# Optimization experiments

Hardware: AMD Instinct MI355X
Metric: run time of the kernel (lower is better)

The kernel has to match this reference:

```python
import jax, jax.numpy as jnp
import numpy as np

NUM_HEADS = 16

def setup_inputs() -> dict:
    key = jax.random.key(0)
    ks = jax.random.split(key, 7)
    B, N, D = 2, 2048, 1024
    x = jax.random.normal(ks[0], (B, N, D), dtype=jnp.float32)
    gamma = jax.random.uniform(ks[1], (B, NUM_HEADS), dtype=jnp.float32)
    dist_matrix = jax.random.uniform(ks[2], (N, N), dtype=jnp.float32)
    W_qkv = jax.random.normal(ks[3], (D, 3 * D), dtype=jnp.float32) * (D ** -0.5)
    b_qkv = jnp.zeros((3 * D,), dtype=jnp.float32)
    W_proj = jax.random.normal(ks[4], (D, D), dtype=jnp.float32) * (D ** -0.5)
    b_proj = jnp.zeros((D,), dtype=jnp.float32)
    return {"x": x, "gamma": gamma, "dist_matrix": dist_matrix,
            "W_qkv": W_qkv, "b_qkv": b_qkv, "W_proj": W_proj, "b_proj": b_proj}

def reference(x, gamma, dist_matrix, W_qkv, b_qkv, W_proj, b_proj):
    B, N, D = x.shape
    H = NUM_HEADS
    hd = D // H
    scale = D ** -0.5  # standard_scale=False -> dim**-0.5
    # qkv projection: [B,N,3D] -> [3,B,H,N,hd]
    qkv = (x @ W_qkv + b_qkv).reshape(B, N, 3, H, hd).transpose(2, 0, 3, 1, 4)
    q, k, v = qkv[0], qkv[1], qkv[2]
    # scores with zoom bias: [B,H,N,N]
    scores = jnp.einsum('bhnd,bhmd->bhnm', q, k) * scale
    scores = scores - gamma[:, :, None, None] * dist_matrix[None, None, :, :]
    attn = jax.nn.softmax(scores, axis=-1)
    out = jnp.einsum('bhnm,bhmd->bhnd', attn, v)  # [B,H,N,hd]
    out = out.transpose(0, 2, 1, 3).reshape(B, N, D)
    return out @ W_proj + b_proj
```

## Files before the change

kernel.cpp:

```cpp
#include <hip/hip_runtime.h>
#include <cstdint>
#include <cstddef>

#define HD 64
#define NH 16
#define BATCH 2
#define SEQ 2048
#define DIM 1024
#define SCALE 0.03125f
#define LOG2E 1.4426950408889634f
#define QSCALE (SCALE * LOG2E)
#define NT (SEQ / 64)

typedef short bf16x8 __attribute__((ext_vector_type(8)));
typedef float f32x4 __attribute__((ext_vector_type(4)));
typedef float f32x16 __attribute__((ext_vector_type(16)));
typedef unsigned u32x4 __attribute__((ext_vector_type(4)));

#define GL16(gp, lp) __builtin_amdgcn_global_load_lds( \
    (const __attribute__((address_space(1))) unsigned int*)(gp), \
    (__attribute__((address_space(3))) unsigned int*)(lp), 16, 0, 0)

static __device__ __forceinline__ unsigned short f2bf(float f) {
  union { float f; unsigned u; } a; a.f = f;
  unsigned r = a.u + 0x7fffu + ((a.u >> 16) & 1u);
  return (unsigned short)(r >> 16);
}

static __device__ __forceinline__ f32x4 zero4() {
  f32x4 z; z[0] = 0.f; z[1] = 0.f; z[2] = 0.f; z[3] = 0.f; return z;
}

__global__ void convert_x(const float* __restrict__ in, unsigned short* __restrict__ out, int n4) {
  int i = blockIdx.x * blockDim.x + threadIdx.x;
  if (i < n4) {
    float4 v = reinterpret_cast<const float4*>(in)[i];
    ushort4 o;
    o.x = f2bf(v.x); o.y = f2bf(v.y); o.z = f2bf(v.z); o.w = f2bf(v.w);
    reinterpret_cast<ushort4*>(out)[i] = o;
  }
}

__global__ void transpose_convert(const float* __restrict__ in, unsigned short* __restrict__ out,
                                  int R, int C) {
  __shared__ float tile[32][33];
  int bx = blockIdx.x * 32;
  int by = blockIdx.y * 32;
  int tx = threadIdx.x, ty = threadIdx.y;
  #pragma unroll
  for (int i = 0; i < 32; i += 8)
    tile[ty + i][tx] = in[(size_t)(by + ty + i) * C + bx + tx];
  __syncthreads();
  #pragma unroll
  for (int i = 0; i < 32; i += 8)
    out[(size_t)(bx + ty + i) * R + by + tx] = f2bf(tile[tx][ty + i]);
}

__global__ __launch_bounds__(256) void gemm128(
    const unsigned short* __restrict__ A, const unsigned short* __restrict__ Bt,
    const float* __restrict__ bias, int K, int mode,
    unsigned short* __restrict__ qo, unsigned short* __restrict__ ko,
    unsigned short* __restrict__ vo, float* __restrict__ outf) {
  __shared__ __attribute__((aligned(16))) unsigned short As[128 * 64];
  __shared__ __attribute__((aligned(16))) unsigned short Bs[128 * 64];
  const int tid = threadIdx.x;
  const int lane = tid & 63, w = tid >> 6;
  const int lo = lane & 15, hi = lane >> 4;
  const int wm = w >> 1, wn = w & 1;
  const int m0 = blockIdx.y * 128, n0 = blockIdx.x * 128;
  const int srow = tid >> 3, scol = (tid & 7) * 8;
  const unsigned short* abase = A + (size_t)(m0 + srow) * K + scol;
  const unsigned short* bbase = Bt + (size_t)(n0 + srow) * K + scol;

  f32x4 acc[4][4];
  #pragma unroll
  for (int mr = 0; mr < 4; ++mr)
    #pragma unroll
    for (int nr = 0; nr < 4; ++nr) acc[mr][nr] = zero4();

  const int nkt = K / 64;
  for (int kt = 0; kt < nkt; ++kt) {
    const unsigned short* ak = abase + kt * 64;
    const unsigned short* bk = bbase + kt * 64;
    #pragma unroll
    for (int i = 0; i < 4; ++i) {
      GL16(ak + (size_t)(32 * i) * K, &As[(w * 64 + 256 * i) * 8]);
      GL16(bk + (size_t)(32 * i) * K, &Bs[(w * 64 + 256 * i) * 8]);
    }
    __syncthreads();
    __builtin_amdgcn_s_setprio(1);
    #pragma unroll
    for (int kc = 0; kc < 2; ++kc) {
      bf16x8 af[4], bfr[4];
      #pragma unroll
      for (int mr = 0; mr < 4; ++mr)
        af[mr] = *reinterpret_cast<const bf16x8*>(
            &As[(wm * 64 + mr * 16 + lo) * 64 + kc * 32 + hi * 8]);
      #pragma unroll
      for (int nr = 0; nr < 4; ++nr)
        bfr[nr] = *reinterpret_cast<const bf16x8*>(
            &Bs[(wn * 64 + nr * 16 + lo) * 64 + kc * 32 + hi * 8]);
      #pragma unroll
      for (int mr = 0; mr < 4; ++mr)
        #pragma unroll
        for (int nr = 0; nr < 4; ++nr)
          acc[mr][nr] = __builtin_amdgcn_mfma_f32_16x16x32_bf16(af[mr], bfr[nr], acc[mr][nr], 0, 0, 0);
    }
    __builtin_amdgcn_s_setprio(0);
    __syncthreads();
  }

  #pragma unroll
  for (int nr = 0; nr < 4; ++nr) {
    const int gcol = n0 + wn * 64 + nr * 16 + lo;
    const float bv = bias[gcol];
    #pragma unroll
    for (int mr = 0; mr < 4; ++mr)
      #pragma unroll
      for (int j = 0; j < 4; ++j) {
        const int grow = m0 + wm * 64 + mr * 16 + hi * 4 + j;
        float val = acc[mr][nr][j] + bv;
        if (mode == 0) {
          int which = gcol >> 10;
          int hh = (gcol >> 6) & 15;
          int d = gcol & 63;
          int bb = grow >> 11;
          int n = grow & 2047;
          if (which == 0) {
            qo[((size_t)(bb * NH + hh) * SEQ + n) * HD + d] = f2bf(val * QSCALE);
          } else if (which == 1) {
            ko[((size_t)(bb * NH + hh) * SEQ + n) * HD + d] = f2bf(val);
          } else {
            vo[((size_t)(bb * NH + hh) * HD + d) * SEQ + n] = f2bf(val);
          }
        } else {
          outf[(size_t)grow * DIM + gcol] = val;
        }
      }
  }
}

__global__ __launch_bounds__(256, 2) void attn_kernel(
    const unsigned short* __restrict__ qb, const unsigned short* __restrict__ kb,
    const unsigned short* __restrict__ vtb, const float* __restrict__ gamma,
    const float* __restrict__ dist, unsigned short* __restrict__ ab) {
  __shared__ __attribute__((aligned(16))) unsigned short Ks[2][64 * 64];
  __shared__ __attribute__((aligned(16))) unsigned short Vt[2][64 * 64];
  const int tid = threadIdx.x;
  const int lane = tid & 63;
  const int w = tid >> 6;
  const int q5 = lane & 31;
  const int h5 = lane >> 5;
  const int idx = blockIdx.x;
  const int bh = idx & 31;
  const int qt = idx >> 5;
  const int b = bh >> 4, h = bh & 15;
  const int qrow0 = qt * 128 + w * 32;
  const float g2 = gamma[bh] * LOG2E;

  const size_t base = (size_t)bh * SEQ * HD;
  const size_t vtbase = (size_t)bh * HD * SEQ;

  bf16x8 qf[4];
  #pragma unroll
  for (int ks = 0; ks < 4; ++ks)
    qf[ks] = *reinterpret_cast<const bf16x8*>(
        &qb[base + (size_t)(qrow0 + q5) * HD + ks * 16 + h5 * 8]);

  const float* drow = dist + (size_t)(qrow0 + q5) * SEQ + 4 * h5;

  f32x16 o[2];
  #pragma unroll
  for (int i = 0; i < 16; ++i) { o[0][i] = 0.f; o[1][i] = 0.f; }
  float m_run = -INFINITY;
  float l_run = 0.f;

  const int srow = tid >> 3;
  const int schunk = (tid & 7) ^ (srow & 7);
  const unsigned short* ksrc0 = kb + base + (size_t)srow * HD + schunk * 8;
  const unsigned short* ksrc1 = ksrc0 + (size_t)32 * HD;
  const unsigned short* vsrc0 = vtb + vtbase + (size_t)srow * SEQ + schunk * 8;
  const unsigned short* vsrc1 = vsrc0 + (size_t)32 * SEQ;

  f32x4 dv[2][4];
  #pragma unroll
  for (int blk = 0; blk < 2; ++blk)
    #pragma unroll
    for (int rp = 0; rp < 4; ++rp)
      dv[blk][rp] = *reinterpret_cast<const f32x4*>(drow + 32 * blk + 8 * rp);

  GL16(ksrc0, &Ks[0][w * 512]);
  GL16(ksrc1, &Ks[0][2048 + w * 512]);
  GL16(vsrc0, &Vt[0][w * 512]);
  GL16(vsrc1, &Vt[0][2048 + w * 512]);
  __syncthreads();

  for (int mt = 0; mt < NT; ++mt) {
    const int cur = mt & 1;
    if (mt + 1 < NT) {
      const int m1 = (mt + 1) * 64;
      GL16(ksrc0 + (size_t)m1 * HD, &Ks[cur ^ 1][w * 512]);
      GL16(ksrc1 + (size_t)m1 * HD, &Ks[cur ^ 1][2048 + w * 512]);
      GL16(vsrc0 + m1, &Vt[cur ^ 1][w * 512]);
      GL16(vsrc1 + m1, &Vt[cur ^ 1][2048 + w * 512]);
    }

    f32x16 s[2];
    #pragma unroll
    for (int i = 0; i < 16; ++i) { s[0][i] = 0.f; s[1][i] = 0.f; }
    __builtin_amdgcn_s_setprio(1);
    #pragma unroll
    for (int blk = 0; blk < 2; ++blk)
      #pragma unroll
      for (int ks = 0; ks < 4; ++ks) {
        bf16x8 kf = *reinterpret_cast<const bf16x8*>(
            &Ks[cur][(blk * 32 + q5) * 64 + ((ks * 2 + h5) ^ (q5 & 7)) * 8]);
        s[blk] = __builtin_amdgcn_mfma_f32_32x32x16_bf16(kf, qf[ks], s[blk], 0, 0, 0);
      }
    __builtin_amdgcn_s_setprio(0);

    float mx[8];
    #pragma unroll
    for (int blk = 0; blk < 2; ++blk)
      #pragma unroll
      for (int rp = 0; rp < 4; ++rp) {
        float v0 = __builtin_fmaf(-g2, dv[blk][rp][0], s[blk][rp * 4 + 0]);
        float v1 = __builtin_fmaf(-g2, dv[blk][rp][1], s[blk][rp * 4 + 1]);
        float v2 = __builtin_fmaf(-g2, dv[blk][rp][2], s[blk][rp * 4 + 2]);
        float v3 = __builtin_fmaf(-g2, dv[blk][rp][3], s[blk][rp * 4 + 3]);
        s[blk][rp * 4 + 0] = v0; s[blk][rp * 4 + 1] = v1;
        s[blk][rp * 4 + 2] = v2; s[blk][rp * 4 + 3] = v3;
        mx[blk * 4 + rp] = fmaxf(fmaxf(v0, v1), fmaxf(v2, v3));
      }
    float pm = fmaxf(fmaxf(fmaxf(mx[0], mx[1]), fmaxf(mx[2], mx[3])),
                     fmaxf(fmaxf(mx[4], mx[5]), fmaxf(mx[6], mx[7])));
    pm = fmaxf(pm, __shfl_xor(pm, 32, 64));

    if (mt + 1 < NT) {
      const float* dn = drow + (mt + 1) * 64;
      #pragma unroll
      for (int blk = 0; blk < 2; ++blk)
        #pragma unroll
        for (int rp = 0; rp < 4; ++rp)
          dv[blk][rp] = *reinterpret_cast<const f32x4*>(dn + 32 * blk + 8 * rp);
    }

    if (!__all(pm <= m_run + 8.0f)) {
      float mn = fmaxf(m_run, pm);
      float corr = exp2f(m_run - mn);
      m_run = mn;
      l_run *= corr;
      #pragma unroll
      for (int i = 0; i < 16; ++i) { o[0][i] *= corr; o[1][i] *= corr; }
    }

    float psum = 0.f;
    unsigned u[2][4][2];
    #pragma unroll
    for (int blk = 0; blk < 2; ++blk)
      #pragma unroll
      for (int rp = 0; rp < 4; ++rp) {
        float p0 = exp2f(s[blk][rp * 4 + 0] - m_run);
        float p1 = exp2f(s[blk][rp * 4 + 1] - m_run);
        float p2 = exp2f(s[blk][rp * 4 + 2] - m_run);
        float p3 = exp2f(s[blk][rp * 4 + 3] - m_run);
        psum += (p0 + p1) + (p2 + p3);
        asm("v_cvt_pk_bf16_f32 %0, %1, %2" : "=v"(u[blk][rp][0]) : "v"(p0), "v"(p1));
        asm("v_cvt_pk_bf16_f32 %0, %1, %2" : "=v"(u[blk][rp][1]) : "v"(p2), "v"(p3));
      }
    psum += __shfl_xor(psum, 32, 64);
    l_run += psum;

    unsigned pu[4][4];
    #pragma unroll
    for (int blk = 0; blk < 2; ++blk)
      #pragma unroll
      for (int jp = 0; jp < 2; ++jp) {
        unsigned a0 = u[blk][0][jp], b0 = u[blk][1][jp];
        asm("v_permlane32_swap_b32 %0, %1" : "+v"(a0), "+v"(b0));
        pu[2 * blk][jp] = a0; pu[2 * blk][2 + jp] = b0;
        unsigned a1 = u[blk][2][jp], b1 = u[blk][3][jp];
        asm("v_permlane32_swap_b32 %0, %1" : "+v"(a1), "+v"(b1));
        pu[2 * blk + 1][jp] = a1; pu[2 * blk + 1][2 + jp] = b1;
      }

    __builtin_amdgcn_s_setprio(1);
    #pragma unroll
    for (int ks = 0; ks < 4; ++ks) {
      u32x4 t; t[0] = pu[ks][0]; t[1] = pu[ks][1]; t[2] = pu[ks][2]; t[3] = pu[ks][3];
      bf16x8 pf = __builtin_bit_cast(bf16x8, t);
      #pragma unroll
      for (int db = 0; db < 2; ++db) {
        bf16x8 vtf = *reinterpret_cast<const bf16x8*>(
            &Vt[cur][(db * 32 + q5) * 64 + ((ks * 2 + h5) ^ (q5 & 7)) * 8]);
        o[db] = __builtin_amdgcn_mfma_f32_32x32x16_bf16(vtf, pf, o[db], 0, 0, 0);
      }
    }
    __builtin_amdgcn_s_setprio(0);

    __syncthreads();
  }

  {
    float rl = 1.0f / l_run;
    size_t row = (size_t)b * SEQ + qrow0 + q5;
    unsigned short* obase = ab + row * DIM + h * HD + 4 * h5;
    #pragma unroll
    for (int db = 0; db < 2; ++db)
      #pragma unroll
      for (int rp = 0; rp < 4; ++rp) {
        ushort4 w4;
        w4.x = f2bf(o[db][rp * 4 + 0] * rl);
        w4.y = f2bf(o[db][rp * 4 + 1] * rl);
        w4.z = f2bf(o[db][rp * 4 + 2] * rl);
        w4.w = f2bf(o[db][rp * 4 + 3] * rl);
        *reinterpret_cast<ushort4*>(&obase[db * 32 + 8 * rp]) = w4;
      }
  }
}

extern "C" void kernel_launch(void* const* d_in, const int* in_sizes, int n_in,
                              void* d_out, int out_size, void* d_ws, size_t ws_size,
                              hipStream_t stream) {
  const float* x     = (const float*)d_in[0];
  const float* gamma = (const float*)d_in[1];
  const float* dist  = (const float*)d_in[2];
  const float* Wqkv  = (const float*)d_in[3];
  const float* bqkv  = (const float*)d_in[4];
  const float* Wproj = (const float*)d_in[5];
  const float* bproj = (const float*)d_in[6];
  float* out = (float*)d_out;

  char* ws = (char*)d_ws;
  unsigned short* xb     = (unsigned short*)(ws);
  unsigned short* wqkvt  = (unsigned short*)(ws + 8388608);
  unsigned short* wprojt = (unsigned short*)(ws + 14680064);
  unsigned short* qbuf   = (unsigned short*)(ws + 16777216);
  unsigned short* kbuf   = (unsigned short*)(ws + 25165824);
  unsigned short* vtbuf  = (unsigned short*)(ws + 33554432);
  unsigned short* abuf   = (unsigned short*)(ws + 41943040);

  convert_x<<<4096, 256, 0, stream>>>(x, xb, (BATCH * SEQ * DIM) / 4);
  transpose_convert<<<dim3(96, 32), dim3(32, 8), 0, stream>>>(Wqkv, wqkvt, DIM, 3 * DIM);
  transpose_convert<<<dim3(32, 32), dim3(32, 8), 0, stream>>>(Wproj, wprojt, DIM, DIM);
  gemm128<<<dim3(24, 32), 256, 0, stream>>>(xb, wqkvt, bqkv, DIM, 0, qbuf, kbuf, vtbuf, nullptr);
  attn_kernel<<<(SEQ / 128) * BATCH * NH, 256, 0, stream>>>(qbuf, kbuf, vtbuf, gamma, dist, abuf);
  gemm128<<<dim3(8, 32), 256, 0, stream>>>(abuf, wprojt, bproj, DIM, 1, nullptr, nullptr, nullptr, out);
}
```

Before: 173.8 us.

## Split attention KV range across two wave groups and swizzle GEMM block order

The attention block grows to 512 threads. Two groups of four waves each handle half of the key/value sequence for the same query rows, using separate double-buffered LDS tiles, and their partial softmax states are merged through LDS at the end. This doubles the number of resident waves working per query tile, which should improve latency hiding in the memory- and exp-bound loop. The cost is more LDS (64KB per block) and an extra combine step. Separately, the GEMM remaps block indices with an XCD-style swizzle so neighbouring tiles land on the same chiplet for better L2 reuse.

New measurement: 217.3 us. +25.0%, slower.

```diff
diff --git a/kernel.cpp b/kernel.cpp
--- a/kernel.cpp
+++ b/kernel.cpp
@@ -10,7 +10,7 @@
 #define SCALE 0.03125f
 #define LOG2E 1.4426950408889634f
 #define QSCALE (SCALE * LOG2E)
-#define NT (SEQ / 64)
+#define NTT 16
 
 typedef short bf16x8 __attribute__((ext_vector_type(8)));
 typedef float f32x4 __attribute__((ext_vector_type(4)));
@@ -67,7 +67,11 @@
   const int lane = tid & 63, w = tid >> 6;
   const int lo = lane & 15, hi = lane >> 4;
   const int wm = w >> 1, wn = w & 1;
-  const int m0 = blockIdx.y * 128, n0 = blockIdx.x * 128;
+  const int gx = gridDim.x;
+  const int nwg = gx * gridDim.y;
+  const int flat = blockIdx.y * gx + blockIdx.x;
+  const int swz = (flat & 7) * (nwg >> 3) + (flat >> 3);
+  const int m0 = (swz / gx) * 128, n0 = (swz % gx) * 128;
   const int srow = tid >> 3, scol = (tid & 7) * 8;
   const unsigned short* abase = A + (size_t)(m0 + srow) * K + scol;
   const unsigned short* bbase = Bt + (size_t)(n0 + srow) * K + scol;
@@ -140,26 +144,30 @@
   }
 }
 
-__global__ __launch_bounds__(256, 2) void attn_kernel(
+__global__ __launch_bounds__(512, 4) void attn_kernel(
     const unsigned short* __restrict__ qb, const unsigned short* __restrict__ kb,
     const unsigned short* __restrict__ vtb, const float* __restrict__ gamma,
     const float* __restrict__ dist, unsigned short* __restrict__ ab) {
-  __shared__ __attribute__((aligned(16))) unsigned short Ks[2][64 * 64];
-  __shared__ __attribute__((aligned(16))) unsigned short Vt[2][64 * 64];
+  __shared__ __attribute__((aligned(16))) unsigned short lds[32768];
   const int tid = threadIdx.x;
   const int lane = tid & 63;
-  const int w = tid >> 6;
+  const int w8 = tid >> 6;
+  const int glw = w8 & 3;
+  const int half = w8 >> 2;
+  const int ltid = tid & 255;
   const int q5 = lane & 31;
   const int h5 = lane >> 5;
   const int idx = blockIdx.x;
   const int bh = idx & 31;
   const int qt = idx >> 5;
   const int b = bh >> 4, h = bh & 15;
-  const int qrow0 = qt * 128 + w * 32;
+  const int qrow0 = qt * 128 + glw * 32;
   const float g2 = gamma[bh] * LOG2E;
 
   const size_t base = (size_t)bh * SEQ * HD;
   const size_t vtbase = (size_t)bh * HD * SEQ;
+
+#define TOF(HALF, KV, BUF) ((((HALF) * 2 + (KV)) * 2 + (BUF)) * 4096)
 
   bf16x8 qf[4];
   #pragma unroll
@@ -167,7 +175,7 @@
     qf[ks] = *reinterpret_cast<const bf16x8*>(
         &qb[base + (size_t)(qrow0 + q5) * HD + ks * 16 + h5 * 8]);
 
-  const float* drow = dist + (size_t)(qrow0 + q5) * SEQ + 4 * h5;
+  const float* drow = dist + (size_t)(qrow0 + q5) * SEQ + half * 1024 + 4 * h5;
 
   f32x16 o[2];
   #pragma unroll
@@ -175,11 +183,11 @@
   float m_run = -INFINITY;
   float l_run = 0.f;
 
-  const int srow = tid >> 3;
-  const int schunk = (tid & 7) ^ (srow & 7);
-  const unsigned short* ksrc0 = kb + base + (size_t)srow * HD + schunk * 8;
+  const int srow = ltid >> 3;
+  const int schunk = (ltid & 7) ^ (srow & 7);
+  const unsigned short* ksrc0 = kb + base + (size_t)(half * 1024 + srow) * HD + schunk * 8;
   const unsigned short* ksrc1 = ksrc0 + (size_t)32 * HD;
-  const unsigned short* vsrc0 = vtb + vtbase + (size_t)srow * SEQ + schunk * 8;
+  const unsigned short* vsrc0 = vtb + vtbase + (size_t)srow * SEQ + half * 1024 + schunk * 8;
   const unsigned short* vsrc1 = vsrc0 + (size_t)32 * SEQ;
 
   f32x4 dv[2][4];
@@ -189,20 +197,20 @@
     for (int rp = 0; rp < 4; ++rp)
       dv[blk][rp] = *reinterpret_cast<const f32x4*>(drow + 32 * blk + 8 * rp);
 
-  GL16(ksrc0, &Ks[0][w * 512]);
-  GL16(ksrc1, &Ks[0][2048 + w * 512]);
-  GL16(vsrc0, &Vt[0][w * 512]);
-  GL16(vsrc1, &Vt[0][2048 + w * 512]);
+  GL16(ksrc0, &lds[TOF(half, 0, 0) + glw * 512]);
+  GL16(ksrc1, &lds[TOF(half, 0, 0) + 2048 + glw * 512]);
+  GL16(vsrc0, &lds[TOF(half, 1, 0) + glw * 512]);
+  GL16(vsrc1, &lds[TOF(half, 1, 0) + 2048 + glw * 512]);
   __syncthreads();
 
-  for (int mt = 0; mt < NT; ++mt) {
+  for (int mt = 0; mt < NTT; ++mt) {
     const int cur = mt & 1;
-    if (mt + 1 < NT) {
+    if (mt + 1 < NTT) {
       const int m1 = (mt + 1) * 64;
-      GL16(ksrc0 + (size_t)m1 * HD, &Ks[cur ^ 1][w * 512]);
-      GL16(ksrc1 + (size_t)m1 * HD, &Ks[cur ^ 1][2048 + w * 512]);
-      GL16(vsrc0 + m1, &Vt[cur ^ 1][w * 512]);
-      GL16(vsrc1 + m1, &Vt[cur ^ 1][2048 + w * 512]);
+      GL16(ksrc0 + (size_t)m1 * HD, &lds[TOF(half, 0, cur ^ 1) + glw * 512]);
+      GL16(ksrc1 + (size_t)m1 * HD, &lds[TOF(half, 0, cur ^ 1) + 2048 + glw * 512]);
+      GL16(vsrc0 + m1, &lds[TOF(half, 1, cur ^ 1) + glw * 512]);
+      GL16(vsrc1 + m1, &lds[TOF(half, 1, cur ^ 1) + 2048 + glw * 512]);
     }
 
     f32x16 s[2];
@@ -214,7 +222,7 @@
       #pragma unroll
       for (int ks = 0; ks < 4; ++ks) {
         bf16x8 kf = *reinterpret_cast<const bf16x8*>(
-            &Ks[cur][(blk * 32 + q5) * 64 + ((ks * 2 + h5) ^ (q5 & 7)) * 8]);
+            &lds[TOF(half, 0, cur) + (blk * 32 + q5) * 64 + ((ks * 2 + h5) ^ (q5 & 7)) * 8]);
         s[blk] = __builtin_amdgcn_mfma_f32_32x32x16_bf16(kf, qf[ks], s[blk], 0, 0, 0);
       }
     __builtin_amdgcn_s_setprio(0);
@@ -236,7 +244,7 @@
                      fmaxf(fmaxf(mx[4], mx[5]), fmaxf(mx[6], mx[7])));
     pm = fmaxf(pm, __shfl_xor(pm, 32, 64));
 
-    if (mt + 1 < NT) {
+    if (mt + 1 < NTT) {
       const float* dn = drow + (mt + 1) * 64;
       #pragma unroll
       for (int blk = 0; blk < 2; ++blk)
@@ -292,7 +300,7 @@
       #pragma unroll
       for (int db = 0; db < 2; ++db) {
         bf16x8 vtf = *reinterpret_cast<const bf16x8*>(
-            &Vt[cur][(db * 32 + q5) * 64 + ((ks * 2 + h5) ^ (q5 & 7)) * 8]);
+            &lds[TOF(half, 1, cur) + (db * 32 + q5) * 64 + ((ks * 2 + h5) ^ (q5 & 7)) * 8]);
         o[db] = __builtin_amdgcn_mfma_f32_32x32x16_bf16(vtf, pf, o[db], 0, 0, 0);
       }
     }
@@ -301,8 +309,20 @@
     __syncthreads();
   }
 
-  {
-    float rl = 1.0f / l_run;
+  float* fx = reinterpret_cast<float*>(lds);
+  const int cslot = (glw * 64 + lane) * 37;
+  if (half == 1) {
+    #pragma unroll
+    for (int i = 0; i < 16; ++i) { fx[cslot + i] = o[0][i]; fx[cslot + 16 + i] = o[1][i]; }
+    fx[cslot + 32] = m_run;
+    fx[cslot + 33] = l_run;
+  }
+  __syncthreads();
+  if (half == 0) {
+    float m1 = fx[cslot + 32], l1 = fx[cslot + 33];
+    float M = fmaxf(m_run, m1);
+    float w0 = exp2f(m_run - M), w1 = exp2f(m1 - M);
+    float rl = 1.0f / (l_run * w0 + l1 * w1);
     size_t row = (size_t)b * SEQ + qrow0 + q5;
     unsigned short* obase = ab + row * DIM + h * HD + 4 * h5;
     #pragma unroll
@@ -310,13 +330,15 @@
       #pragma unroll
       for (int rp = 0; rp < 4; ++rp) {
         ushort4 w4;
-        w4.x = f2bf(o[db][rp * 4 + 0] * rl);
-        w4.y = f2bf(o[db][rp * 4 + 1] * rl);
-        w4.z = f2bf(o[db][rp * 4 + 2] * rl);
-        w4.w = f2bf(o[db][rp * 4 + 3] * rl);
+        #pragma unroll
+        for (int j = 0; j < 4; ++j) {
+          float comb = (o[db][rp * 4 + j] * w0 + fx[cslot + db * 16 + rp * 4 + j] * w1) * rl;
+          reinterpret_cast<unsigned short*>(&w4)[j] = f2bf(comb);
+        }
         *reinterpret_cast<ushort4*>(&obase[db * 32 + 8 * rp]) = w4;
       }
   }
+#undef TOF
 }
 
 extern "C" void kernel_launch(void* const* d_in, const int* in_sizes, int n_in,
@@ -344,6 +366,6 @@
   transpose_convert<<<dim3(96, 32), dim3(32, 8), 0, stream>>>(Wqkv, wqkvt, DIM, 3 * DIM);
   transpose_convert<<<dim3(32, 32), dim3(32, 8), 0, stream>>>(Wproj, wprojt, DIM, DIM);
   gemm128<<<dim3(24, 32), 256, 0, stream>>>(xb, wqkvt, bqkv, DIM, 0, qbuf, kbuf, vtbuf, nullptr);
-  attn_kernel<<<(SEQ / 128) * BATCH * NH, 256, 0, stream>>>(qbuf, kbuf, vtbuf, gamma, dist, abuf);
+  attn_kernel<<<(SEQ / 128) * BATCH * NH, 512, 0, stream>>>(qbuf, kbuf, vtbuf, gamma, dist, abuf);
   gemm128<<<dim3(8, 32), 256, 0, stream>>>(abuf, wprojt, bproj, DIM, 1, nullptr, nullptr, nullptr, out);
 }
```
